# Kernel tuning notes

Measured on AMD Instinct MI355X. Metric: run time of the kernel, lower is better.

Reference implementation:

```python
import jax, jax.numpy as jnp
import numpy as np

KH, KW = 3, 3
K = KH * KW
PAD, STRIDE, DIL = 1, 1, 1


def _conv(x, w, b):
    y = jax.lax.conv_general_dilated(
        x, w, (STRIDE, STRIDE), ((PAD, PAD), (PAD, PAD)),
        rhs_dilation=(DIL, DIL), dimension_numbers=('NCHW', 'OIHW', 'NCHW'))
    return y + b[None, :, None, None]


def _bilinear_gather(x, py, px):
    # x: [B,C,H,W]; py, px: float sample coords [B,K,Ho,Wo]. Zero outside bounds.
    B, C, H, W = x.shape
    y0 = jnp.floor(py)
    x0 = jnp.floor(px)
    wy1 = py - y0
    wx1 = px - x0
    wy0 = 1.0 - wy1
    wx0 = 1.0 - wx1
    xf = x.reshape(B, C, H * W)

    def g(yi, xi):
        valid = (yi >= 0) & (yi < H) & (xi >= 0) & (xi < W)
        yc = jnp.clip(yi, 0, H - 1).astype(jnp.int32)
        xc = jnp.clip(xi, 0, W - 1).astype(jnp.int32)
        idx = (yc * W + xc).reshape(B, -1)                      # [B, K*Ho*Wo]
        v = jax.vmap(lambda im, ix: im[:, ix])(xf, idx)         # [B, C, K*Ho*Wo]
        v = v.reshape(B, C, *yi.shape[1:])                      # [B,C,K,Ho,Wo]
        return v * valid[:, None].astype(x.dtype)

    return ((wy0 * wx0)[:, None] * g(y0, x0)
            + (wy0 * wx1)[:, None] * g(y0, x0 + 1)
            + (wy1 * wx0)[:, None] * g(y0 + 1, x0)
            + (wy1 * wx1)[:, None] * g(y0 + 1, x0 + 1))


def setup_inputs() -> dict:
    key = jax.random.key(0)
    k1, k2, k3 = jax.random.split(key, 3)
    B, C, H, W = 8, 256, 64, 64
    x = jax.random.normal(k1, (B, C, H, W), dtype=jnp.float32)
    # small init for offset/mask conv so predicted offsets stay modest (as in DCNv2 practice)
    w_om = jax.random.normal(k2, (3 * K, C, KH, KW), dtype=jnp.float32) * 0.01
    b_om = jnp.zeros((3 * K,), dtype=jnp.float32)
    w_dc = jax.random.normal(k3, (C, C, KH, KW), dtype=jnp.float32) * (1.0 / np.sqrt(C * K))
    b_dc = jnp.zeros((C,), dtype=jnp.float32)
    return {"x": x, "w_om": w_om, "b_om": b_om, "w_dc": w_dc, "b_dc": b_dc}


def reference(x, w_om, b_om, w_dc, b_dc):
    B, C, H, W = x.shape
    om = _conv(x, w_om, b_om)                      # [B, 3K, H, W]
    offset = om[:, :2 * K].reshape(B, K, 2, H, W)  # per-tap (dy, dx)
    mask = jax.nn.sigmoid(om[:, 2 * K:])           # [B, K, H, W]
    dy, dx = offset[:, :, 0], offset[:, :, 1]
    kh = jnp.repeat(jnp.arange(KH), KW)            # [K] kernel row index
    kw = jnp.tile(jnp.arange(KW), KH)              # [K] kernel col index
    ho = jnp.arange(H)
    wo = jnp.arange(W)
    py = ho[None, None, :, None] * STRIDE - PAD + kh[None, :, None, None] * DIL + dy
    px = wo[None, None, None, :] * STRIDE - PAD + kw[None, :, None, None] * DIL + dx
    sampled = _bilinear_gather(x, py, px)          # [B,C,K,H,W]
    sampled = sampled * mask[:, None]              # modulated (DCNv2)
    w = w_dc.reshape(w_dc.shape[0], C, K)
    out = jnp.einsum('bckhw,ock->bohw', sampled, w) + b_dc[None, :, None, None]
    return out
```

## Files before the change

### kernel.cpp

```cpp
#include <hip/hip_runtime.h>
#include <hip/hip_bf16.h>
#include <hip/hip_fp16.h>
#include <math.h>

#define BB   8
#define CIN  256
#define HH   64
#define WW   64
#define OMC  27
#define HW   (HH*WW)
#define KTOT (CIN*9)
#define NPIX 32
#define SPITCH 296
#define XP1    40
#define TPW    17

typedef short bf16x8 __attribute__((ext_vector_type(8)));
typedef float f32x4  __attribute__((ext_vector_type(4)));

__device__ __forceinline__ unsigned short f2bf(float f) {
    union { float f; unsigned int u; } v; v.f = f;
    unsigned int r = v.u + 0x7FFFu + ((v.u >> 16) & 1u);
    return (unsigned short)(r >> 16);
}
__device__ __forceinline__ unsigned int pk2bf(float a, float b) {
    union { __hip_bfloat162 h; unsigned int u; } c;
    c.h = __float22bfloat162_rn(make_float2(a, b));
    return c.u;
}
__device__ __forceinline__ float bflo(unsigned int a) {
    union { unsigned int u; float f; } c; c.u = a << 16; return c.f;
}
__device__ __forceinline__ float bfhi(unsigned int a) {
    union { unsigned int u; float f; } c; c.u = a & 0xFFFF0000u; return c.f;
}

__global__ __launch_bounds__(256) void prep_kernel(
    const float* __restrict__ w_dc, const float* __restrict__ w_om,
    unsigned short* __restrict__ wA, unsigned short* __restrict__ wOmA)
{
    int bid = blockIdx.x;
    if (bid < 2304) {
        int e = bid * 256 + threadIdx.x;
        int o = e / KTOT;
        int k = e - o * KTOT;
        int c   = k / 9;
        int tap = k - c * 9;
        int kp  = (c >> 5) * 288 + tap * 32 + (c & 31);
        wA[((size_t)(kp >> 3) * 256 + o) * 8 + (kp & 7)] = f2bf(w_dc[e]);
    } else {
        int e = (bid - 2304) * 256 + threadIdx.x;
        int j  = e & 7;
        int t1 = e >> 3;
        int o  = t1 & 31;
        int t2 = t1 >> 5;
        int cb = t2 & 3;
        int t3 = t2 >> 2;
        int cc = t3 & 7;
        int tap = t3 >> 3;
        int c = cc * 32 + cb * 8 + j;
        float v = (o < OMC) ? w_om[(size_t)o * KTOT + c * 9 + tap] : 0.f;
        wOmA[e] = f2bf(v);
    }
}

__global__ __launch_bounds__(512, 4) void om_mfma_kernel(
    const float* __restrict__ x, const unsigned short* __restrict__ wOmA,
    const float* __restrict__ b_om, float* __restrict__ om)
{
    const int rawb = blockIdx.x;
    const int obid = ((rawb & 7) << 7) | (rawb >> 3);
    const int b    = obid >> 7;
    const int h    = (obid >> 1) & 63;
    const int w0   = (obid & 1) * 32;
    const int t    = threadIdx.x;
    const int wv   = t >> 6;
    const int lane = t & 63;
    const int lq   = lane >> 4;
    const int lm   = lane & 15;
    const int mfp  = (wv >> 1) & 1;
    const int nfp  = wv & 1;
    const int p    = nfp * 16 + lm;

    __shared__ __align__(16) unsigned short sX[2 * 102 * XP1];

    unsigned short* bufA = sX;
    unsigned short* bufB = sX + 102 * XP1;

    const size_t xb_base = (size_t)b * CIN * HW;
    const float* gx_base = x + xb_base;
    const bf16x8* wOmV = reinterpret_cast<const bf16x8*>(wOmA);

    f32x4 accOm = (f32x4)(0.f);

    auto stage1 = [&](int cc, unsigned short* dst) {
        const float* gch = gx_base + (size_t)cc * 32 * HW;
#pragma unroll
        for (int i = 0; i < 7; ++i) {
            int e = t + i * 512;
            if (e < 102 * 32) {
                int cl  = e / 102;
                int rc  = e - cl * 102;
                int row = rc / 34;
                int col = rc - row * 34;
                int gy  = h - 1 + row;
                int gxx = w0 - 1 + col;
                float v = 0.f;
                if (gy >= 0 && gy < HH && (unsigned)gxx < WW)
                    v = gch[cl * HW + gy * WW + gxx];
                dst[rc * XP1 + cl] = f2bf(v);
            }
        }
    };

    stage1(0, bufA);
    __syncthreads();
    for (int ch = 0; ch < 8; ++ch) {
        unsigned short* cur = (ch & 1) ? bufB : bufA;
        unsigned short* nxt = (ch & 1) ? bufA : bufB;
        if (ch < 7) stage1(ch + 1, nxt);
#pragma unroll
        for (int tap = 0; tap < 9; ++tap) {
            int th = tap / 3, tw = tap % 3;
            bf16x8 bfr = *reinterpret_cast<const bf16x8*>(
                &cur[(th * 34 + p + tw) * XP1 + lq * 8]);
            bf16x8 af = wOmV[(((tap * 8 + ch) * 4 + lq) * 32) + mfp * 16 + lm];
            accOm = __builtin_amdgcn_mfma_f32_16x16x32_bf16(af, bfr, accOm, 0, 0, 0);
        }
        __syncthreads();
    }

    if (wv < 4) {
#pragma unroll
        for (int r = 0; r < 4; ++r) {
            int o = mfp * 16 + lq * 4 + r;
            if (o < OMC)
                om[((size_t)(b * OMC + o) * HH + h) * WW + w0 + p] =
                    accOm[r] + b_om[o];
        }
    }
}

__global__ __launch_bounds__(512, 4) void deform_mfma_kernel(
    const float* __restrict__ x, const float* __restrict__ om,
    const unsigned short* __restrict__ wA, const float* __restrict__ b_dc,
    float* __restrict__ out)
{
    const int rawb = blockIdx.x;
    const int obid = ((rawb & 7) << 7) | (rawb >> 3);
    const int b    = obid >> 7;
    const int h    = (obid >> 1) & 63;
    const int w0   = (obid & 1) * NPIX;
    const int t    = threadIdx.x;
    const int wv   = t >> 6;
    const int lane = t & 63;
    const int lq   = lane >> 4;
    const int lm   = lane & 15;

    __shared__ __align__(16) unsigned short sS[NPIX * SPITCH];
    __shared__ __align__(16) unsigned short sR[8224];
    __shared__ __align__(16) int4 s_par[9 * NPIX];

    const size_t xb_base = (size_t)b * CIN * HW;
    const float* gx_base = x + xb_base;

    int stg[7];
#pragma unroll
    for (int i = 0; i < 7; ++i) {
        int n = t + i * 512;
        if (n < 3200) {
            int slot = n / 200;
            int rc   = n - slot * 200;
            int r    = rc / 40;
            int c    = rc - r * 40;
            int gy   = min(max(h - 2 + r, 0), HH - 1);
            int gx   = min(max(w0 - 4 + c, 0), WW - 1);
            stg[i] = (rc * TPW + slot) | (slot << 12) | ((gy * WW + gx) << 16);
        } else stg[i] = -1;
    }

    unsigned int* tWw = reinterpret_cast<unsigned int*>(sR);
    const unsigned int* tW = tWw;

    float L0[7], L1[7];
    {
        const float* gch = gx_base;
#pragma unroll
        for (int i = 0; i < 7; ++i)
            if (stg[i] >= 0) {
                int sl = (stg[i] >> 12) & 0xF;
                int go = (stg[i] >> 16) & 0xFFF;
                L0[i] = gch[(size_t)(2 * sl) * HW + go];
                L1[i] = gch[(size_t)(2 * sl + 1) * HW + go];
            }
    }

    for (int i = t; i < 712; i += 512) tWw[3400 + i] = 0u;

    if (t < 9 * NPIX) {
        int tap = t >> 5;
        int pix = t & 31;
        const float* omb = om + ((size_t)b * OMC * HH + h) * WW + w0 + pix;
        float dy = omb[(size_t)(2 * tap) * HW];
        float dx = omb[(size_t)(2 * tap + 1) * HW];
        float mv = omb[(size_t)(18 + tap) * HW];
        float m  = 1.f / (1.f + expf(-mv));
        float py = (float)(h - 1 + tap / 3) + dy;
        float px = (float)(w0 + pix - 1 + tap % 3) + dx;
        float y0f = floorf(py), x0f = floorf(px);
        float wy1 = py - y0f, wx1 = px - x0f;
        float wy0 = 1.f - wy1, wx0 = 1.f - wx1;
        int y0 = (int)y0f, x0 = (int)x0f;
        int y1 = y0 + 1, x1 = x0 + 1;
        bool yv0 = (y0 >= 0) && (y0 < HH);
        bool yv1 = (y1 >= 0) && (y1 < HH);
        bool xv0 = (x0 >= 0) && (x0 < WW);
        bool xv1 = (x1 >= 0) && (x1 < WW);
        int yc0 = min(max(y0, 0), HH - 1), yc1 = min(max(y1, 0), HH - 1);
        int xc0 = min(max(x0, 0), WW - 1), xc1 = min(max(x1, 0), WW - 1);
        float wwx = (yv0 && xv0) ? wy0 * wx0 * m : 0.f;
        float wwy = (yv0 && xv1) ? wy0 * wx1 * m : 0.f;
        float wwz = (yv1 && xv0) ? wy1 * wx0 * m : 0.f;
        float www = (yv1 && xv1) ? wy1 * wx1 * m : 0.f;
        if (xc1 == xc0) { wwx += wwy; wwy = 0.f; wwz += www; www = 0.f; }
        if (yc1 == yc0) { wwx += wwz; wwz = 0.f; wwy += www; www = 0.f; }
        bool inT = (yc0 >= h - 2) && (yc1 <= h + 2) &&
                   (xc0 >= w0 - 4) && (xc1 <= w0 + 35);
        int lb = (yc0 - (h - 2)) * 40 + (xc0 - (w0 - 4));
        int pk = (lb & 0xFF) | ((xc1 - xc0) << 8) | ((yc1 - yc0) << 9)
               | ((yc0 * WW + xc0) << 10);
        if (!inT) pk |= (int)0x80000000;
        __half2 wab = __floats2half2_rn(wwx, wwy);
        __half2 wcd = __floats2half2_rn(wwz, www);
        s_par[t] = make_int4(pk,
                             *reinterpret_cast<int*>(&wab),
                             *reinterpret_cast<int*>(&wcd), 0);
    }
    {
#pragma unroll
        for (int i = 0; i < 7; ++i)
            if (stg[i] >= 0)
                tWw[stg[i] & 0xFFF] = pk2bf(L0[i], L1[i]);
    }
    __syncthreads();

    f32x4 acc[2][2];
#pragma unroll
    for (int i = 0; i < 2; ++i)
#pragma unroll
        for (int j = 0; j < 2; ++j)
            acc[i][j] = (f32x4)(0.f);

    const int pix  = t >> 4;
    const int slot = t & 15;

    for (int ch = 0; ch < 8; ++ch) {
#pragma unroll 3
        for (int tap = 0; tap < 9; ++tap) {
            int idx = tap * NPIX + pix;
            int4 pv = s_par[idx];
            int pk  = pv.x;
            float2 wab = __half22float2(*reinterpret_cast<__half2*>(&pv.y));
            float2 wcd = __half22float2(*reinterpret_cast<__half2*>(&pv.z));
            float v0, v1;
            if (pk >= 0) {
                int base = (pk & 0xFF) * TPW + slot;
                unsigned int a00 = tW[base];
                unsigned int a01 = tW[base + TPW];
                unsigned int a10 = tW[base + 40 * TPW];
                unsigned int a11 = tW[base + 41 * TPW];
                v0 = wab.x * bflo(a00) + wab.y * bflo(a01)
                   + wcd.x * bflo(a10) + wcd.y * bflo(a11);
                v1 = wab.x * bfhi(a00) + wab.y * bfhi(a01)
                   + wcd.x * bfhi(a10) + wcd.y * bfhi(a11);
            } else {
                int off00 = (pk >> 10) & 0xFFF;
                int d01 = (pk >> 8) & 1;
                int d10 = ((pk >> 9) & 1) * WW;
                const float* xc = x + xb_base + (size_t)(ch * 32 + 2 * slot) * HW;
                v0 = wab.x * xc[off00]       + wab.y * xc[off00 + d01]
                   + wcd.x * xc[off00 + d10] + wcd.y * xc[off00 + d10 + d01];
                xc += HW;
                v1 = wab.x * xc[off00]       + wab.y * xc[off00 + d01]
                   + wcd.x * xc[off00 + d10] + wcd.y * xc[off00 + d10 + d01];
            }
            *reinterpret_cast<unsigned int*>(
                &sS[pix * SPITCH + tap * 32 + 2 * slot]) = pk2bf(v0, v1);
        }
        __syncthreads();

        if (ch < 7) {
            const float* gch = gx_base + (size_t)(ch + 1) * 32 * HW;
#pragma unroll
            for (int i = 0; i < 7; ++i)
                if (stg[i] >= 0) {
                    int sl = (stg[i] >> 12) & 0xF;
                    int go = (stg[i] >> 16) & 0xFFF;
                    L0[i] = gch[(size_t)(2 * sl) * HW + go];
                    L1[i] = gch[(size_t)(2 * sl + 1) * HW + go];
                }
        }

        const int kb_base = ch * 36;
        const bf16x8* wAv = reinterpret_cast<const bf16x8*>(wA);
#pragma unroll 1
        for (int ks = 0; ks < 9; ++ks) {
            bf16x8 bfr[2];
#pragma unroll
            for (int nf = 0; nf < 2; ++nf)
                bfr[nf] = *reinterpret_cast<const bf16x8*>(
                    &sS[(nf * 16 + lm) * SPITCH + ks * 32 + lq * 8]);
#pragma unroll
            for (int mf = 0; mf < 2; ++mf) {
                int o  = wv * 32 + mf * 16 + lm;
                int kb = kb_base + ks * 4 + lq;
                bf16x8 af = wAv[(size_t)kb * 256 + o];
#pragma unroll
                for (int nf = 0; nf < 2; ++nf)
                    acc[mf][nf] = __builtin_amdgcn_mfma_f32_16x16x32_bf16(
                        af, bfr[nf], acc[mf][nf], 0, 0, 0);
            }
        }

        if (ch < 7) {
#pragma unroll
            for (int i = 0; i < 7; ++i)
                if (stg[i] >= 0)
                    tWw[stg[i] & 0xFFF] = pk2bf(L0[i], L1[i]);
        }
        __syncthreads();
    }

#pragma unroll
    for (int mf = 0; mf < 2; ++mf) {
#pragma unroll
        for (int r = 0; r < 4; ++r) {
            int o = wv * 32 + mf * 16 + lq * 4 + r;
            float bo = b_dc[o];
#pragma unroll
            for (int nf = 0; nf < 2; ++nf) {
                int p = nf * 16 + lm;
                out[((size_t)(b * 256 + o)) * HW + h * WW + w0 + p] = acc[mf][nf][r] + bo;
            }
        }
    }
}

extern "C" void kernel_launch(void* const* d_in, const int* in_sizes, int n_in,
                              void* d_out, int out_size, void* d_ws, size_t ws_size,
                              hipStream_t stream) {
    const float* x    = (const float*)d_in[0];
    const float* w_om = (const float*)d_in[1];
    const float* b_om = (const float*)d_in[2];
    const float* w_dc = (const float*)d_in[3];
    const float* b_dc = (const float*)d_in[4];
    float* out = (float*)d_out;

    unsigned short* wA   = (unsigned short*)d_ws;
    unsigned short* wOmA = (unsigned short*)((char*)d_ws + 1179648);
    float*          om   = (float*)((char*)d_ws + 1327104);

    prep_kernel<<<2304 + 288, 256, 0, stream>>>(w_dc, w_om, wA, wOmA);
    om_mfma_kernel<<<BB * HH * 2, 512, 0, stream>>>(x, wOmA, b_om, om);
    deform_mfma_kernel<<<BB * HH * 2, 512, 0, stream>>>(x, om, wA, b_dc, out);
}
```

Measured before the change: 153.1 us.

## Split offset-conv channel reduction across two wave groups with LDS reduction

The offset/mask conv kernel previously had all 8 waves work on the same 4 MFMA tiles, with 4 of the 8 waves doing redundant work. Now the waves form two groups, each covering half of the input-channel chunks with its own double buffer. The two partial sums are then combined through shared memory before the store. This doubles LDS use and adds a reduction barrier, and each group stages its own tiles with 256 threads instead of 512.

```diff
diff --git a/kernel.cpp b/kernel.cpp
--- a/kernel.cpp
+++ b/kernel.cpp
@@ -75,17 +75,21 @@
     const int w0   = (obid & 1) * 32;
     const int t    = threadIdx.x;
     const int wv   = t >> 6;
+    const int grp  = wv >> 2;
+    const int tg   = t & 255;
     const int lane = t & 63;
     const int lq   = lane >> 4;
     const int lm   = lane & 15;
-    const int mfp  = (wv >> 1) & 1;
-    const int nfp  = wv & 1;
+    const int wg   = wv & 3;
+    const int mfp  = (wg >> 1) & 1;
+    const int nfp  = wg & 1;
     const int p    = nfp * 16 + lm;
 
-    __shared__ __align__(16) unsigned short sX[2 * 102 * XP1];
-
-    unsigned short* bufA = sX;
-    unsigned short* bufB = sX + 102 * XP1;
+    __shared__ __align__(16) unsigned short sX[4 * 102 * XP1];
+    float* som_tmp = reinterpret_cast<float*>(sX);
+
+    unsigned short* bufA = sX + grp * 2 * (102 * XP1);
+    unsigned short* bufB = bufA + 102 * XP1;
 
     const size_t xb_base = (size_t)b * CIN * HW;
     const float* gx_base = x + xb_base;
@@ -93,11 +97,11 @@
 
     f32x4 accOm = (f32x4)(0.f);
 
-    auto stage1 = [&](int cc, unsigned short* dst) {
+    auto stage1g = [&](int cc, unsigned short* dst) {
         const float* gch = gx_base + (size_t)cc * 32 * HW;
 #pragma unroll
-        for (int i = 0; i < 7; ++i) {
-            int e = t + i * 512;
+        for (int i = 0; i < 13; ++i) {
+            int e = tg + i * 256;
             if (e < 102 * 32) {
                 int cl  = e / 102;
                 int rc  = e - cl * 102;
@@ -113,12 +117,13 @@
         }
     };
 
-    stage1(0, bufA);
+    stage1g(grp * 4, bufA);
     __syncthreads();
-    for (int ch = 0; ch < 8; ++ch) {
-        unsigned short* cur = (ch & 1) ? bufB : bufA;
-        unsigned short* nxt = (ch & 1) ? bufA : bufB;
-        if (ch < 7) stage1(ch + 1, nxt);
+    for (int q = 0; q < 4; ++q) {
+        const int ch = grp * 4 + q;
+        unsigned short* cur = (q & 1) ? bufB : bufA;
+        unsigned short* nxt = (q & 1) ? bufA : bufB;
+        if (q < 3) stage1g(ch + 1, nxt);
 #pragma unroll
         for (int tap = 0; tap < 9; ++tap) {
             int th = tap / 3, tw = tap % 3;
@@ -130,13 +135,22 @@
         __syncthreads();
     }
 
-    if (wv < 4) {
+    if (grp == 1) {
+#pragma unroll
+        for (int r = 0; r < 4; ++r) {
+            int o = mfp * 16 + lq * 4 + r;
+            if (o < 32)
+                som_tmp[o * 32 + p] = accOm[r];
+        }
+    }
+    __syncthreads();
+    if (grp == 0) {
 #pragma unroll
         for (int r = 0; r < 4; ++r) {
             int o = mfp * 16 + lq * 4 + r;
             if (o < OMC)
                 om[((size_t)(b * OMC + o) * HH + h) * WW + w0 + p] =
-                    accOm[r] + b_om[o];
+                    accOm[r] + som_tmp[o * 32 + p] + b_om[o];
         }
     }
 }
```

After: 149.9 us, median of 2. -2.1%, faster.
